# Performance work log

Measured on AMD Instinct MI355X. Metric: run time of the kernel, lower is better.

The kernel has to match this reference:

```python
import jax, jax.numpy as jnp
import numpy as np


def _safe_pow(v, p):
    # mimic torch.nan_to_num(pow(v, p), nan=0, posinf=0, neginf=0) for v >= 0
    out = jnp.where(v > 0, jnp.power(jnp.where(v > 0, v, 1.0), p), 0.0)
    return out.astype(jnp.float32)


def setup_inputs() -> dict:
    key = jax.random.key(0)
    k1, k2, k3 = jax.random.split(key, 3)
    N, E, Din, Dout = 20000, 4096, 128, 128
    x = jax.random.normal(k1, (N, Din), dtype=jnp.float32)
    H = jax.random.uniform(k2, (N, E), dtype=jnp.float32)
    W = jax.random.normal(k3, (Dout, Din), dtype=jnp.float32) * (1.0 / np.sqrt(Din))
    b = jnp.zeros((Dout,), dtype=jnp.float32)
    return {"x": x, "H": H, "W": W, "b": b}


def reference(x, H, W, b):
    # Dv^{-1/2}: node degrees; De^{-1}: hyperedge degrees.
    # torch.diag(...)**p with nan/inf->0 is exactly diagonal scaling, so we
    # use broadcasted vector scaling fused around the two GEMMs.
    dv = _safe_pow(jnp.sum(H, axis=-1), -0.5)   # [N]
    de = _safe_pow(jnp.sum(H, axis=0), -1.0)    # [E]
    x = dv[:, None] * x                          # Dv^{-1/2} x
    x = H.T @ x                                  # [E, Din]
    x = de[:, None] * x                          # De^{-1}
    x = H @ x                                    # [N, Din]
    x = dv[:, None] * x                          # Dv^{-1/2}
    return x @ W.T + b                           # Linear
```

## Files before the change

### kernel.cpp

```cpp
#include <hip/hip_runtime.h>
#include <hip/hip_bf16.h>
#include <stdint.h>


#define N_ 20000
#define E_ 4096
#define D_ 128
#define XTB_S 20032
#define SPLIT 8

typedef __attribute__((ext_vector_type(8))) short    bf16x8;
typedef __attribute__((ext_vector_type(4))) float    f32x4;
typedef __attribute__((ext_vector_type(8))) unsigned short us8;
typedef __attribute__((ext_vector_type(4))) unsigned short us4;

__device__ __forceinline__ unsigned short f2bf(float f) {
  unsigned u = __float_as_uint(f);
  u += 0x7FFFu + ((u >> 16) & 1u);
  return (unsigned short)(u >> 16);
}
__device__ __forceinline__ unsigned cvtpk(float lo, float hi) {
  unsigned r;
  asm("v_cvt_pk_bf16_f32 %0, %1, %2" : "=v"(r) : "v"(lo), "v"(hi));
  return r;
}
__device__ __forceinline__ void gload16(const unsigned short* g, unsigned short* l) {
  __builtin_amdgcn_global_load_lds(
      (const __attribute__((address_space(1))) unsigned int*)g,
      (__attribute__((address_space(3))) unsigned int*)l, 16, 0, 0);
}

__global__ __launch_bounds__(256) void k_pre(const float* __restrict__ H,
                                             const float* __restrict__ x,
                                             float* __restrict__ dv,
                                             unsigned short* __restrict__ Hb,
                                             unsigned short* __restrict__ xTb) {
  const int t = threadIdx.x, lane = t & 63, w = t >> 6;
  const int b = blockIdx.x;
  if (b >= 2500) {
    const size_t base = (size_t)(20000 + (b - 2500) * 8) * E_;
    for (int i = t; i < 4096; i += 256)
      *(us8*)&Hb[base + (size_t)i * 8] = (us8){0,0,0,0,0,0,0,0};
    if (b == 2500 && t < 128) {
#pragma unroll
      for (int c = 0; c < 4; ++c)
        *(us8*)&xTb[(size_t)t * XTB_S + 20000 + c * 8] = (us8){0,0,0,0,0,0,0,0};
    }
    return;
  }
  __shared__ float red[32];
  __shared__ float xt[8 * 128];
  const int n0 = b * 8;
  { int r = t >> 5, d4 = (t & 31) * 4;
    *(f32x4*)&xt[r * 128 + d4] = *(const f32x4*)(x + (size_t)(n0 + r) * D_ + d4); }
  float rs[8];
#pragma unroll
  for (int r = 0; r < 8; ++r) {
    rs[r] = 0.f;
    const float* rp = H + (size_t)(n0 + r) * E_;
    unsigned short* hp = Hb + (size_t)(n0 + r) * E_;
#pragma unroll
    for (int j = 0; j < 4; ++j) {
      f32x4 v = *(const f32x4*)(rp + j * 1024 + t * 4);
      rs[r] += (v.x + v.y) + (v.z + v.w);
      union { us4 v4; unsigned u32[2]; } un;
      un.u32[0] = cvtpk(v.x, v.y);
      un.u32[1] = cvtpk(v.z, v.w);
      *(us4*)(hp + j * 1024 + t * 4) = un.v4;
    }
  }
#pragma unroll
  for (int r = 0; r < 8; ++r)
#pragma unroll
    for (int off = 32; off; off >>= 1) rs[r] += __shfl_xor(rs[r], off);
  if (lane == 0) {
#pragma unroll
    for (int r = 0; r < 8; ++r) red[w * 8 + r] = rs[r];
  }
  __syncthreads();
  if (t < 8) {
    float s = red[t] + red[8 + t] + red[16 + t] + red[24 + t];
    float d = s > 0.f ? rsqrtf(s) : 0.f;
    dv[n0 + t] = d;
    red[t] = d;
  }
  __syncthreads();
  if (t < 128) {
    int d = t;
    float v[8];
#pragma unroll
    for (int r = 0; r < 8; ++r) v[r] = xt[r * 128 + d] * red[r];
    union { us8 v8; unsigned u32[4]; } un;
#pragma unroll
    for (int j = 0; j < 4; ++j) un.u32[j] = cvtpk(v[2 * j], v[2 * j + 1]);
    *(us8*)(xTb + (size_t)d * XTB_S + n0) = un.v8;
  }
}

__global__ __launch_bounds__(256) void k_gemm1(const unsigned short* __restrict__ Hb,
                                               const unsigned short* __restrict__ xTb,
                                               float* __restrict__ partialT,
                                               float* __restrict__ desumP) {
  __shared__ unsigned short lH[2][64 * 64];
  __shared__ unsigned short lX[2][128 * 64];
  const int t = threadIdx.x, lane = t & 63, w = t >> 6;
  const int eb = blockIdx.x & 63, s = blockIdx.x >> 6;
  const int e0 = eb * 64;
  const int nsteps = 39 + (s == 7);
  const int g0 = s * 39;
  const int lrow = lane >> 3, lslot = lane & 7;
  const int bswz = (lslot ^ lrow) << 3;
  const int wy = w >> 1, wx = w & 1;
  const int ep = t & 31, q = t >> 5;
  const int er0 = 2 * ep, er1 = 2 * ep + 1;
  const int sl0 = (q ^ (er0 & 7)) << 3, sl1 = (q ^ (er1 & 7)) << 3;

  f32x4 acc[4][2];
  f32x4 accC[2];
#pragma unroll
  for (int i = 0; i < 4; ++i)
#pragma unroll
    for (int j = 0; j < 2; ++j) acc[i][j] = (f32x4){0.f, 0.f, 0.f, 0.f};
  accC[0] = (f32x4){0.f, 0.f, 0.f, 0.f};
  accC[1] = (f32x4){0.f, 0.f, 0.f, 0.f};
  bf16x8 ones;
#pragma unroll
  for (int i = 0; i < 8; ++i) ones[i] = (short)0x3F80;

  unsigned hr[8];
  auto LOADH = [&](int g) {
    const unsigned short* p = Hb + (size_t)(g * 64 + q * 8) * E_ + e0 + er0;
#pragma unroll
    for (int j = 0; j < 8; ++j) hr[j] = *(const unsigned*)(p + (size_t)j * E_);
  };
  auto WRITEH = [&](int bufi) {
    union { bf16x8 v; unsigned u[4]; } lo, hi;
#pragma unroll
    for (int p = 0; p < 4; ++p) {
      lo.u[p] = (hr[2 * p] & 0xFFFFu) | (hr[2 * p + 1] << 16);
      hi.u[p] = (hr[2 * p] >> 16) | (hr[2 * p + 1] & 0xFFFF0000u);
    }
    *(bf16x8*)&lH[bufi][er0 * 64 + sl0] = lo.v;
    *(bf16x8*)&lH[bufi][er1 * 64 + sl1] = hi.v;
  };
  auto GLOADX = [&](int g, int bufi) {
#pragma unroll
    for (int i = 0; i < 4; ++i) {
      int c = w * 4 + i;
      gload16(xTb + (size_t)(8 * c + lrow) * XTB_S + g * 64 + bswz,
              &lX[bufi][c * 512]);
    }
  };

  LOADH(g0); GLOADX(g0, 0); WRITEH(0);
  __syncthreads();
  int cur = 0;
  for (int it = 0; it < nsteps; ++it) {
    bool hn = it + 1 < nsteps;
    if (hn) { LOADH(g0 + it + 1); GLOADX(g0 + it + 1, cur ^ 1); }
    const int kg = lane >> 4, fr = lane & 15;
    bf16x8 ax[4][2], bh[2][2];
#pragma unroll
    for (int mi = 0; mi < 4; ++mi) {
      int m = wy * 64 + mi * 16 + fr;
#pragma unroll
      for (int kk = 0; kk < 2; ++kk)
        ax[mi][kk] = *(const bf16x8*)&lX[cur][m * 64 + (((kk * 4 + kg) ^ (m & 7)) << 3)];
    }
#pragma unroll
    for (int ni = 0; ni < 2; ++ni) {
      int n = wx * 32 + ni * 16 + fr;
#pragma unroll
      for (int kk = 0; kk < 2; ++kk)
        bh[ni][kk] = *(const bf16x8*)&lH[cur][n * 64 + (((kk * 4 + kg) ^ (n & 7)) << 3)];
    }
#pragma unroll
    for (int kk = 0; kk < 2; ++kk)
#pragma unroll
      for (int mi = 0; mi < 4; ++mi)
#pragma unroll
        for (int ni = 0; ni < 2; ++ni)
          acc[mi][ni] = __builtin_amdgcn_mfma_f32_16x16x32_bf16(ax[mi][kk], bh[ni][kk], acc[mi][ni], 0, 0, 0);
    if (wy == 0) {
#pragma unroll
      for (int kk = 0; kk < 2; ++kk)
#pragma unroll
        for (int ni = 0; ni < 2; ++ni)
          accC[ni] = __builtin_amdgcn_mfma_f32_16x16x32_bf16(ones, bh[ni][kk], accC[ni], 0, 0, 0);
    }
    if (hn) WRITEH(cur ^ 1);
    __syncthreads();
    cur ^= 1;
  }
  const int kg = lane >> 4, fr = lane & 15;
  if (wy == 0 && kg == 0) {
#pragma unroll
    for (int ni = 0; ni < 2; ++ni)
      desumP[s * E_ + e0 + wx * 32 + ni * 16 + fr] = accC[ni][0];
  }
#pragma unroll
  for (int mi = 0; mi < 4; ++mi)
#pragma unroll
    for (int ni = 0; ni < 2; ++ni)
#pragma unroll
      for (int r = 0; r < 4; ++r) {
        int d = wy * 64 + mi * 16 + kg * 4 + r;
        int e = e0 + wx * 32 + ni * 16 + fr;
        partialT[((size_t)s * 128 + d) * E_ + e] = acc[mi][ni][r];
      }
}

__global__ __launch_bounds__(256) void k_reduce1(const float* __restrict__ partialT,
                                                 const float* __restrict__ desumP,
                                                 unsigned short* __restrict__ x3T) {
  int tid = blockIdx.x * 256 + threadIdx.x;
  int d = tid >> 9;
  int e0 = (tid & 511) * 8;
  f32x4 sA = {0.f,0.f,0.f,0.f}, sB = {0.f,0.f,0.f,0.f};
  f32x4 dA = {0.f,0.f,0.f,0.f}, dB = {0.f,0.f,0.f,0.f};
#pragma unroll
  for (int ss = 0; ss < SPLIT; ++ss) {
    const float* p = partialT + ((size_t)ss * 128 + d) * E_ + e0;
    sA += *(const f32x4*)p;
    sB += *(const f32x4*)(p + 4);
    const float* qd = desumP + ss * E_ + e0;
    dA += *(const f32x4*)qd;
    dB += *(const f32x4*)(qd + 4);
  }
  float sv[8] = {sA.x, sA.y, sA.z, sA.w, sB.x, sB.y, sB.z, sB.w};
  float dvv[8] = {dA.x, dA.y, dA.z, dA.w, dB.x, dB.y, dB.z, dB.w};
  float o[8];
#pragma unroll
  for (int i = 0; i < 8; ++i)
    o[i] = dvv[i] > 0.f ? sv[i] / dvv[i] : 0.f;
  union { us8 v8; unsigned u32[4]; } un;
#pragma unroll
  for (int j = 0; j < 4; ++j) un.u32[j] = cvtpk(o[2 * j], o[2 * j + 1]);
  *(us8*)(x3T + (size_t)d * E_ + e0) = un.v8;
}

__global__ __launch_bounds__(256) void k_gemm2(const unsigned short* __restrict__ Hb,
                                               const unsigned short* __restrict__ x3T,
                                               const float* __restrict__ W,
                                               const float* __restrict__ dv,
                                               const float* __restrict__ bias,
                                               float* __restrict__ out) {
  __shared__ unsigned short sm[2 * 64 * 64 + 2 * 128 * 64];
  __shared__ unsigned short lW[128 * 128];
  unsigned short (*lA)[64 * 64]  = (unsigned short (*)[64 * 64])sm;
  unsigned short (*lB)[128 * 64] = (unsigned short (*)[128 * 64])(sm + 2 * 64 * 64);
  unsigned short* lC = sm;
  const int t = threadIdx.x, lane = t & 63, w = t >> 6;
  const int n0b = blockIdx.x * 64;
  const int lrow = lane >> 3, lslot = lane & 7;
  const int bswz = (lslot ^ lrow) << 3;
  const int wy = w >> 1, wx = w & 1;

  {
    int j = t >> 1;
    int sb = (t & 1) * 8;
#pragma unroll
    for (int jj = 0; jj < 4; ++jj) {
      int s0 = sb + jj * 2;
      const float* wp = W + (size_t)j * 128 + s0 * 8;
      f32x4 a = *(const f32x4*)wp,       b4 = *(const f32x4*)(wp + 4);
      f32x4 c = *(const f32x4*)(wp + 8), d4 = *(const f32x4*)(wp + 12);
      union { us8 v; unsigned u[4]; } u0, u1;
      u0.u[0] = cvtpk(a.x, a.y);   u0.u[1] = cvtpk(a.z, a.w);
      u0.u[2] = cvtpk(b4.x, b4.y); u0.u[3] = cvtpk(b4.z, b4.w);
      u1.u[0] = cvtpk(c.x, c.y);   u1.u[1] = cvtpk(c.z, c.w);
      u1.u[2] = cvtpk(d4.x, d4.y); u1.u[3] = cvtpk(d4.z, d4.w);
      *(us8*)&lW[j * 128 + ((s0 ^ (j & 7)) << 3)]       = u0.v;
      *(us8*)&lW[j * 128 + (((s0 + 1) ^ (j & 7)) << 3)] = u1.v;
    }
  }

  auto GLOADA = [&](int g, int bufi) {
#pragma unroll
    for (int i = 0; i < 2; ++i) {
      int c = w * 2 + i;
      gload16(Hb + (size_t)(n0b + 8 * c + lrow) * E_ + g * 64 + bswz,
              &lA[bufi][c * 512]);
    }
  };
  auto GLOADB = [&](int g, int bufi) {
#pragma unroll
    for (int i = 0; i < 4; ++i) {
      int c = w * 4 + i;
      gload16(x3T + (size_t)(8 * c + lrow) * E_ + g * 64 + bswz,
              &lB[bufi][c * 512]);
    }
  };

  f32x4 acc[2][4];
#pragma unroll
  for (int i = 0; i < 2; ++i)
#pragma unroll
    for (int j = 0; j < 4; ++j) acc[i][j] = (f32x4){0.f, 0.f, 0.f, 0.f};

  GLOADA(0, 0); GLOADB(0, 0);
  __syncthreads();
  int cur = 0;
  for (int it = 0; it < 64; ++it) {
    bool hn = it < 63;
    if (hn) { GLOADA(it + 1, cur ^ 1); GLOADB(it + 1, cur ^ 1); }
    const int kg = lane >> 4, fr = lane & 15;
    bf16x8 af[2][2], bfr[4][2];
#pragma unroll
    for (int mi = 0; mi < 2; ++mi) {
      int m = wy * 32 + mi * 16 + fr;
#pragma unroll
      for (int kk = 0; kk < 2; ++kk)
        af[mi][kk] = *(const bf16x8*)&lA[cur][m * 64 + (((kk * 4 + kg) ^ (m & 7)) << 3)];
    }
#pragma unroll
    for (int ni = 0; ni < 4; ++ni) {
      int d = wx * 64 + ni * 16 + fr;
#pragma unroll
      for (int kk = 0; kk < 2; ++kk)
        bfr[ni][kk] = *(const bf16x8*)&lB[cur][d * 64 + (((kk * 4 + kg) ^ (d & 7)) << 3)];
    }
#pragma unroll
    for (int kk = 0; kk < 2; ++kk)
#pragma unroll
      for (int mi = 0; mi < 2; ++mi)
#pragma unroll
        for (int ni = 0; ni < 4; ++ni)
          acc[mi][ni] = __builtin_amdgcn_mfma_f32_16x16x32_bf16(af[mi][kk], bfr[ni][kk], acc[mi][ni], 0, 0, 0);
    __syncthreads();
    cur ^= 1;
  }
#pragma unroll
  for (int mi = 0; mi < 2; ++mi) {
    float dvv[4];
#pragma unroll
    for (int r = 0; r < 4; ++r)
      dvv[r] = dv[min(n0b + wy * 32 + mi * 16 + (lane >> 4) * 4 + r, N_ - 1)];
#pragma unroll
    for (int ni = 0; ni < 4; ++ni)
#pragma unroll
      for (int r = 0; r < 4; ++r) {
        int row = wy * 32 + mi * 16 + (lane >> 4) * 4 + r;
        int col = wx * 64 + ni * 16 + (lane & 15);
        lC[row * 136 + col] = f2bf(acc[mi][ni][r] * dvv[r]);
      }
  }
  __syncthreads();
  f32x4 acc2[2][4];
#pragma unroll
  for (int i = 0; i < 2; ++i)
#pragma unroll
    for (int j = 0; j < 4; ++j) acc2[i][j] = (f32x4){0.f, 0.f, 0.f, 0.f};
#pragma unroll
  for (int ks = 0; ks < 4; ++ks) {
    const int kg = lane >> 4, fr = lane & 15;
    int kofs = ks * 32 + kg * 8;
    bf16x8 a2[2], b2[4];
#pragma unroll
    for (int mi = 0; mi < 2; ++mi) {
      int m = wy * 32 + mi * 16 + fr;
      a2[mi] = *(const bf16x8*)&lC[m * 136 + kofs];
    }
#pragma unroll
    for (int ni = 0; ni < 4; ++ni) {
      int j2 = wx * 64 + ni * 16 + fr;
      b2[ni] = *(const bf16x8*)&lW[j2 * 128 + (((ks * 4 + kg) ^ (j2 & 7)) << 3)];
    }
#pragma unroll
    for (int mi = 0; mi < 2; ++mi)
#pragma unroll
      for (int ni = 0; ni < 4; ++ni)
        acc2[mi][ni] = __builtin_amdgcn_mfma_f32_16x16x32_bf16(a2[mi], b2[ni], acc2[mi][ni], 0, 0, 0);
  }
#pragma unroll
  for (int mi = 0; mi < 2; ++mi)
#pragma unroll
    for (int ni = 0; ni < 4; ++ni) {
      int j2 = wx * 64 + ni * 16 + (lane & 15);
      float bb = bias[j2];
#pragma unroll
      for (int r = 0; r < 4; ++r) {
        int n = n0b + wy * 32 + mi * 16 + (lane >> 4) * 4 + r;
        if (n < N_) out[(size_t)n * D_ + j2] = acc2[mi][ni][r] + bb;
      }
    }
}

extern "C" void kernel_launch(void* const* d_in, const int* in_sizes, int n_in,
                              void* d_out, int out_size, void* d_ws, size_t ws_size,
                              hipStream_t stream) {
  const float* x = (const float*)d_in[0];
  const float* H = (const float*)d_in[1];
  const float* W = (const float*)d_in[2];
  const float* b = (const float*)d_in[3];
  float* out = (float*)d_out;
  char* ws = (char*)d_ws;
  float*          desumP   = (float*)(ws);
  float*          dv       = (float*)(ws + 131072);
  unsigned short* xTb      = (unsigned short*)(ws + 211200);
  unsigned short* x3T      = (unsigned short*)(ws + 5339392);
  float*          partialT = (float*)(ws + 6387968);
  unsigned short* Hb       = (unsigned short*)(ws + 23165184);

  k_pre<<<2504, 256, 0, stream>>>(H, x, dv, Hb, xTb);
  k_gemm1<<<512, 256, 0, stream>>>(Hb, xTb, partialT, desumP);
  k_reduce1<<<256, 256, 0, stream>>>(partialT, desumP, x3T);
  k_gemm2<<<313, 256, 0, stream>>>(Hb, x3T, W, dv, b, out);
}
```

Measured before the change: 235.9 us.

## Apply Linear weight to the small E-side product and raise gemm1 split-K

The Linear layer W is now applied by reassociation: the reduction kernel multiplies the De-scaled [E,128] intermediate by W (an MFMA GEMM over E rows only). gemm2 therefore outputs the final result with just dv scaling and bias, which drops the per-tile second GEMM over N rows and the W staging in LDS. The gemm1 split-K factor also goes from 8 to 12 (768 blocks) so more CUs are busy, with uneven split boundaries. The cost is more partial sums to write and reduce, plus an extra bf16 rounding of the W-transformed intermediate.

New measurement: 224.0 us. 5.0% less time.

```diff
diff --git a/kernel.cpp b/kernel.cpp
--- a/kernel.cpp
+++ b/kernel.cpp
@@ -7,7 +7,7 @@
 #define E_ 4096
 #define D_ 128
 #define XTB_S 20032
-#define SPLIT 8
+#define SPLIT 12
 
 typedef __attribute__((ext_vector_type(8))) short    bf16x8;
 typedef __attribute__((ext_vector_type(4))) float    f32x4;
@@ -32,9 +32,11 @@
 
 __global__ __launch_bounds__(256) void k_pre(const float* __restrict__ H,
                                              const float* __restrict__ x,
+                                             const float* __restrict__ W,
                                              float* __restrict__ dv,
                                              unsigned short* __restrict__ Hb,
-                                             unsigned short* __restrict__ xTb) {
+                                             unsigned short* __restrict__ xTb,
+                                             unsigned short* __restrict__ Wb) {
   const int t = threadIdx.x, lane = t & 63, w = t >> 6;
   const int b = blockIdx.x;
   if (b >= 2500) {
@@ -45,6 +47,18 @@
 #pragma unroll
       for (int c = 0; c < 4; ++c)
         *(us8*)&xTb[(size_t)t * XTB_S + 20000 + c * 8] = (us8){0,0,0,0,0,0,0,0};
+    }
+    if (b == 2501) {
+      int base2 = t * 64;
+#pragma unroll
+      for (int i = 0; i < 8; ++i) {
+        const float* wp = W + base2 + i * 8;
+        f32x4 a = *(const f32x4*)wp, b4 = *(const f32x4*)(wp + 4);
+        union { us8 v; unsigned u[4]; } un;
+        un.u[0] = cvtpk(a.x, a.y);   un.u[1] = cvtpk(a.z, a.w);
+        un.u[2] = cvtpk(b4.x, b4.y); un.u[3] = cvtpk(b4.z, b4.w);
+        *(us8*)(Wb + base2 + i * 8) = un.v;
+      }
     }
     return;
   }
@@ -106,8 +120,8 @@
   const int t = threadIdx.x, lane = t & 63, w = t >> 6;
   const int eb = blockIdx.x & 63, s = blockIdx.x >> 6;
   const int e0 = eb * 64;
-  const int nsteps = 39 + (s == 7);
-  const int g0 = s * 39;
+  const int g0 = (s * 313) / SPLIT;
+  const int g1 = ((s + 1) * 313) / SPLIT;
   const int lrow = lane >> 3, lslot = lane & 7;
   const int bswz = (lslot ^ lrow) << 3;
   const int wy = w >> 1, wx = w & 1;
@@ -155,9 +169,9 @@
   LOADH(g0); GLOADX(g0, 0); WRITEH(0);
   __syncthreads();
   int cur = 0;
-  for (int it = 0; it < nsteps; ++it) {
-    bool hn = it + 1 < nsteps;
-    if (hn) { LOADH(g0 + it + 1); GLOADX(g0 + it + 1, cur ^ 1); }
+  for (int it = g0; it < g1; ++it) {
+    bool hn = it + 1 < g1;
+    if (hn) { LOADH(it + 1); GLOADX(it + 1, cur ^ 1); }
     const int kg = lane >> 4, fr = lane & 15;
     bf16x8 ax[4][2], bh[2][2];
 #pragma unroll
@@ -210,71 +224,92 @@
       }
 }
 
-__global__ __launch_bounds__(256) void k_reduce1(const float* __restrict__ partialT,
-                                                 const float* __restrict__ desumP,
-                                                 unsigned short* __restrict__ x3T) {
-  int tid = blockIdx.x * 256 + threadIdx.x;
-  int d = tid >> 9;
-  int e0 = (tid & 511) * 8;
-  f32x4 sA = {0.f,0.f,0.f,0.f}, sB = {0.f,0.f,0.f,0.f};
-  f32x4 dA = {0.f,0.f,0.f,0.f}, dB = {0.f,0.f,0.f,0.f};
-#pragma unroll
-  for (int ss = 0; ss < SPLIT; ++ss) {
-    const float* p = partialT + ((size_t)ss * 128 + d) * E_ + e0;
-    sA += *(const f32x4*)p;
-    sB += *(const f32x4*)(p + 4);
-    const float* qd = desumP + ss * E_ + e0;
-    dA += *(const f32x4*)qd;
-    dB += *(const f32x4*)(qd + 4);
-  }
-  float sv[8] = {sA.x, sA.y, sA.z, sA.w, sB.x, sB.y, sB.z, sB.w};
-  float dvv[8] = {dA.x, dA.y, dA.z, dA.w, dB.x, dB.y, dB.z, dB.w};
-  float o[8];
-#pragma unroll
-  for (int i = 0; i < 8; ++i)
-    o[i] = dvv[i] > 0.f ? sv[i] / dvv[i] : 0.f;
-  union { us8 v8; unsigned u32[4]; } un;
-#pragma unroll
-  for (int j = 0; j < 4; ++j) un.u32[j] = cvtpk(o[2 * j], o[2 * j + 1]);
-  *(us8*)(x3T + (size_t)d * E_ + e0) = un.v8;
+__global__ __launch_bounds__(256) void k_mid(const float* __restrict__ partialT,
+                                             const float* __restrict__ desumP,
+                                             const unsigned short* __restrict__ Wb,
+                                             unsigned short* __restrict__ x3WT) {
+  __shared__ unsigned short lW[128 * 136];
+  __shared__ unsigned short lE[16 * 132];
+  __shared__ float lT[128 * 20];
+  const int t = threadIdx.x, lane = t & 63, w = t >> 6;
+  const int e0 = blockIdx.x * 16;
+
+  {
+    int j = t >> 1, half = (t & 1) * 64;
+    const us8* src = (const us8*)(Wb + (size_t)j * 128 + half);
+#pragma unroll
+    for (int i = 0; i < 8; ++i)
+      *(us8*)&lW[j * 136 + half + 8 * i] = src[i];
+  }
+  {
+    const int e = e0 + (t & 15);
+    const int d0 = (t >> 4) * 8;
+    float des = 0.f;
+#pragma unroll
+    for (int s = 0; s < SPLIT; ++s) des += desumP[s * E_ + e];
+    float dei = des > 0.f ? 1.f / des : 0.f;
+    float accp[8];
+#pragma unroll
+    for (int i = 0; i < 8; ++i) accp[i] = 0.f;
+#pragma unroll
+    for (int s = 0; s < SPLIT; ++s) {
+      const float* p = partialT + ((size_t)s * 128 + d0) * E_ + e;
+#pragma unroll
+      for (int i = 0; i < 8; ++i) accp[i] += p[(size_t)i * E_];
+    }
+    union { bf16x8 v; unsigned u[4]; } un;
+#pragma unroll
+    for (int i = 0; i < 4; ++i)
+      un.u[i] = cvtpk(accp[2 * i] * dei, accp[2 * i + 1] * dei);
+    *(bf16x8*)&lE[(t & 15) * 132 + d0] = un.v;
+  }
+  __syncthreads();
+  const int kg = lane >> 4, fr = lane & 15;
+  f32x4 acc[2];
+  acc[0] = (f32x4){0.f, 0.f, 0.f, 0.f};
+  acc[1] = (f32x4){0.f, 0.f, 0.f, 0.f};
+#pragma unroll
+  for (int kk = 0; kk < 4; ++kk) {
+    bf16x8 bfrag = *(const bf16x8*)&lE[fr * 132 + (kk * 4 + kg) * 8];
+#pragma unroll
+    for (int mi = 0; mi < 2; ++mi) {
+      int m = w * 32 + mi * 16 + fr;
+      bf16x8 afrag = *(const bf16x8*)&lW[m * 136 + (kk * 4 + kg) * 8];
+      acc[mi] = __builtin_amdgcn_mfma_f32_16x16x32_bf16(afrag, bfrag, acc[mi], 0, 0, 0);
+    }
+  }
+  __syncthreads();
+#pragma unroll
+  for (int mi = 0; mi < 2; ++mi)
+#pragma unroll
+    for (int r = 0; r < 4; ++r)
+      lT[(w * 32 + mi * 16 + kg * 4 + r) * 20 + fr] = acc[mi][r];
+  __syncthreads();
+  {
+    int j = t >> 1, eh = (t & 1) * 8;
+    float v[8];
+#pragma unroll
+    for (int i = 0; i < 8; ++i) v[i] = lT[j * 20 + eh + i];
+    union { us8 v8; unsigned u[4]; } un;
+#pragma unroll
+    for (int i = 0; i < 4; ++i) un.u[i] = cvtpk(v[2 * i], v[2 * i + 1]);
+    *(us8*)(x3WT + (size_t)j * E_ + e0 + eh) = un.v8;
+  }
 }
 
 __global__ __launch_bounds__(256) void k_gemm2(const unsigned short* __restrict__ Hb,
-                                               const unsigned short* __restrict__ x3T,
-                                               const float* __restrict__ W,
+                                               const unsigned short* __restrict__ x3WT,
                                                const float* __restrict__ dv,
                                                const float* __restrict__ bias,
                                                float* __restrict__ out) {
-  __shared__ unsigned short sm[2 * 64 * 64 + 2 * 128 * 64];
-  __shared__ unsigned short lW[128 * 128];
-  unsigned short (*lA)[64 * 64]  = (unsigned short (*)[64 * 64])sm;
-  unsigned short (*lB)[128 * 64] = (unsigned short (*)[128 * 64])(sm + 2 * 64 * 64);
-  unsigned short* lC = sm;
+  __shared__ unsigned short lA[2][64 * 64];
+  __shared__ unsigned short lB[2][128 * 64];
   const int t = threadIdx.x, lane = t & 63, w = t >> 6;
   const int n0b = blockIdx.x * 64;
   const int lrow = lane >> 3, lslot = lane & 7;
   const int bswz = (lslot ^ lrow) << 3;
   const int wy = w >> 1, wx = w & 1;
 
-  {
-    int j = t >> 1;
-    int sb = (t & 1) * 8;
-#pragma unroll
-    for (int jj = 0; jj < 4; ++jj) {
-      int s0 = sb + jj * 2;
-      const float* wp = W + (size_t)j * 128 + s0 * 8;
-      f32x4 a = *(const f32x4*)wp,       b4 = *(const f32x4*)(wp + 4);
-      f32x4 c = *(const f32x4*)(wp + 8), d4 = *(const f32x4*)(wp + 12);
-      union { us8 v; unsigned u[4]; } u0, u1;
-      u0.u[0] = cvtpk(a.x, a.y);   u0.u[1] = cvtpk(a.z, a.w);
-      u0.u[2] = cvtpk(b4.x, b4.y); u0.u[3] = cvtpk(b4.z, b4.w);
-      u1.u[0] = cvtpk(c.x, c.y);   u1.u[1] = cvtpk(c.z, c.w);
-      u1.u[2] = cvtpk(d4.x, d4.y); u1.u[3] = cvtpk(d4.z, d4.w);
-      *(us8*)&lW[j * 128 + ((s0 ^ (j & 7)) << 3)]       = u0.v;
-      *(us8*)&lW[j * 128 + (((s0 + 1) ^ (j & 7)) << 3)] = u1.v;
-    }
-  }
-
   auto GLOADA = [&](int g, int bufi) {
 #pragma unroll
     for (int i = 0; i < 2; ++i) {
@@ -287,7 +322,7 @@
 #pragma unroll
     for (int i = 0; i < 4; ++i) {
       int c = w * 4 + i;
-      gload16(x3T + (size_t)(8 * c + lrow) * E_ + g * 64 + bswz,
+      gload16(x3WT + (size_t)(8 * c + lrow) * E_ + g * 64 + bswz,
               &lB[bufi][c * 512]);
     }
   };
@@ -330,60 +365,24 @@
     __syncthreads();
     cur ^= 1;
   }
+  const int kg = lane >> 4, fr = lane & 15;
 #pragma unroll
   for (int mi = 0; mi < 2; ++mi) {
     float dvv[4];
 #pragma unroll
     for (int r = 0; r < 4; ++r)
-      dvv[r] = dv[min(n0b + wy * 32 + mi * 16 + (lane >> 4) * 4 + r, N_ - 1)];
-#pragma unroll
-    for (int ni = 0; ni < 4; ++ni)
-#pragma unroll
-      for (int r = 0; r < 4; ++r) {
-        int row = wy * 32 + mi * 16 + (lane >> 4) * 4 + r;
-        int col = wx * 64 + ni * 16 + (lane & 15);
-        lC[row * 136 + col] = f2bf(acc[mi][ni][r] * dvv[r]);
-      }
-  }
-  __syncthreads();
-  f32x4 acc2[2][4];
-#pragma unroll
-  for (int i = 0; i < 2; ++i)
-#pragma unroll
-    for (int j = 0; j < 4; ++j) acc2[i][j] = (f32x4){0.f, 0.f, 0.f, 0.f};
-#pragma unroll
-  for (int ks = 0; ks < 4; ++ks) {
-    const int kg = lane >> 4, fr = lane & 15;
-    int kofs = ks * 32 + kg * 8;
-    bf16x8 a2[2], b2[4];
-#pragma unroll
-    for (int mi = 0; mi < 2; ++mi) {
-      int m = wy * 32 + mi * 16 + fr;
-      a2[mi] = *(const bf16x8*)&lC[m * 136 + kofs];
-    }
+      dvv[r] = dv[min(n0b + wy * 32 + mi * 16 + kg * 4 + r, N_ - 1)];
 #pragma unroll
     for (int ni = 0; ni < 4; ++ni) {
       int j2 = wx * 64 + ni * 16 + fr;
-      b2[ni] = *(const bf16x8*)&lW[j2 * 128 + (((ks * 4 + kg) ^ (j2 & 7)) << 3)];
-    }
-#pragma unroll
-    for (int mi = 0; mi < 2; ++mi)
-#pragma unroll
-      for (int ni = 0; ni < 4; ++ni)
-        acc2[mi][ni] = __builtin_amdgcn_mfma_f32_16x16x32_bf16(a2[mi], b2[ni], acc2[mi][ni], 0, 0, 0);
-  }
-#pragma unroll
-  for (int mi = 0; mi < 2; ++mi)
-#pragma unroll
-    for (int ni = 0; ni < 4; ++ni) {
-      int j2 = wx * 64 + ni * 16 + (lane & 15);
       float bb = bias[j2];
 #pragma unroll
       for (int r = 0; r < 4; ++r) {
-        int n = n0b + wy * 32 + mi * 16 + (lane >> 4) * 4 + r;
-        if (n < N_) out[(size_t)n * D_ + j2] = acc2[mi][ni][r] + bb;
+        int n = n0b + wy * 32 + mi * 16 + kg * 4 + r;
+        if (n < N_) out[(size_t)n * D_ + j2] = acc[mi][ni][r] * dvv[r] + bb;
       }
     }
+  }
 }
 
 extern "C" void kernel_launch(void* const* d_in, const int* in_sizes, int n_in,
@@ -396,14 +395,15 @@
   float* out = (float*)d_out;
   char* ws = (char*)d_ws;
   float*          desumP   = (float*)(ws);
-  float*          dv       = (float*)(ws + 131072);
-  unsigned short* xTb      = (unsigned short*)(ws + 211200);
-  unsigned short* x3T      = (unsigned short*)(ws + 5339392);
-  float*          partialT = (float*)(ws + 6387968);
-  unsigned short* Hb       = (unsigned short*)(ws + 23165184);
-
-  k_pre<<<2504, 256, 0, stream>>>(H, x, dv, Hb, xTb);
-  k_gemm1<<<512, 256, 0, stream>>>(Hb, xTb, partialT, desumP);
-  k_reduce1<<<256, 256, 0, stream>>>(partialT, desumP, x3T);
-  k_gemm2<<<313, 256, 0, stream>>>(Hb, x3T, W, dv, b, out);
-}
+  float*          dv       = (float*)(ws + 196608);
+  unsigned short* Wb       = (unsigned short*)(ws + 276736);
+  unsigned short* xTb      = (unsigned short*)(ws + 309504);
+  unsigned short* x3WT     = (unsigned short*)(ws + 5437696);
+  float*          partialT = (float*)(ws + 6486272);
+  unsigned short* Hb       = (unsigned short*)(ws + 31652096);
+
+  k_pre<<<2504, 256, 0, stream>>>(H, x, W, dv, Hb, xTb, Wb);
+  k_gemm1<<<768, 256, 0, stream>>>(Hb, xTb, partialT, desumP);
+  k_mid<<<256, 256, 0, stream>>>(partialT, desumP, Wb, x3WT);
+  k_gemm2<<<313, 256, 0, stream>>>(Hb, x3WT, dv, b, out);
+}
```
